# Optimization experiments

Hardware: AMD Instinct MI355X
Metric: run time of the kernel (lower is better)

## Reference

```python
import jax, jax.numpy as jnp
import numpy as np
from jax import lax

N, OC, IC, K = 32, 256, 256, 3
H = W = 56
STRIDE = 1
PADDING = 1
SPARSITY = 0.9  # fraction of zero weights


def setup_inputs() -> dict:
    key = jax.random.key(0)
    k_in, k_w, k_b, k_m = jax.random.split(key, 4)
    input = jax.random.normal(k_in, (N, IC, H, W), dtype=jnp.float32)
    weight = jax.random.normal(k_w, (OC, IC, K, K), dtype=jnp.float32) * 0.05
    bias = jax.random.normal(k_b, (OC,), dtype=jnp.float32) * 0.05
    mask = jax.random.bernoulli(k_m, p=1.0 - SPARSITY, shape=(OC, IC, K, K))
    return {"input": input, "weight": weight, "bias": bias, "mask": mask}


def reference(input, weight, bias, mask):
    # SparseConv2d stores only nonzero weights (W_val at W_idx); mathematically this
    # is a dense conv2d with the masked weight tensor.
    w = jnp.where(mask, weight, jnp.zeros((), dtype=weight.dtype))
    out = lax.conv_general_dilated(
        input, w,
        window_strides=(STRIDE, STRIDE),
        padding=[(PADDING, PADDING), (PADDING, PADDING)],
        dimension_numbers=("NCHW", "OIHW", "NCHW"),
    )
    return out + bias[None, :, None, None]
```

## Files before the change

kernel.cpp:

```cpp
#include <hip/hip_runtime.h>

constexpr int NB=32, ICC=256, OCC=256, HH=56, WW=56;
constexpr int HW=HH*WW, CHW=ICC*HW;
constexpr int YT=14, MT=2;
constexpr int BUFB = 6*56*64;
constexpr int ZOFF = 2*BUFB;
constexpr int LROW=58;
constexpr int PAD=36;
constexpr int LDS_ELEMS=6*LROW*PAD;

using short8  = __attribute__((ext_vector_type(8))) short;
using short4v = __attribute__((ext_vector_type(4))) short;
using f32x4   = __attribute__((ext_vector_type(4))) float;

__device__ inline unsigned bf16rne(float x){
  unsigned u = __float_as_uint(x);
  return (u + 0x7fffu + ((u>>16)&1u)) >> 16;
}

__global__ __launch_bounds__(256) void pack_weights(
    const float* __restrict__ w, const int* __restrict__ mask,
    unsigned short* __restrict__ wb){
  const int oc = blockIdx.x, ic = threadIdx.x;
  const int base = (oc*ICC + ic)*9;
  #pragma unroll
  for (int j=0;j<9;++j){
    float v = (mask[base+j] != 0) ? w[base+j] : 0.f;
    wb[(j*OCC + oc)*ICC + ic] = (unsigned short)bf16rne(v);
  }
}

__global__ __launch_bounds__(256) void pack_input(
    const float* __restrict__ in, unsigned short* __restrict__ inb){
  __shared__ unsigned short t[56*258];
  const int bid = blockIdx.x;
  const int n = bid/56, y = bid - n*56;
  const float* src = in + (size_t)n*CHW + y*WW;
  const int tid = threadIdx.x;
  #pragma unroll
  for (int i=0;i<14;++i){
    int idx = tid + i*256;
    int ic = idx / 14, xg = idx - ic*14;
    float4 v = *(const float4*)(src + ic*HW + xg*4);
    int xb = xg*4;
    t[(xb+0)*258 + ic] = (unsigned short)bf16rne(v.x);
    t[(xb+1)*258 + ic] = (unsigned short)bf16rne(v.y);
    t[(xb+2)*258 + ic] = (unsigned short)bf16rne(v.z);
    t[(xb+3)*258 + ic] = (unsigned short)bf16rne(v.w);
  }
  __syncthreads();
  unsigned* dst = (unsigned*)(inb + (size_t)(n*56+y)*56*256);
  #pragma unroll
  for (int i=0;i<28;++i){
    int idx = tid + i*256;
    int x = idx >> 7, icp = idx & 127;
    dst[idx] = *(const unsigned*)&t[x*258 + icp*2];
  }
}

__global__ __launch_bounds__(256,2) void conv_mfma(
    const unsigned short* __restrict__ inb, const unsigned short* __restrict__ wb,
    const float* __restrict__ bias, float* __restrict__ out){
  __shared__ unsigned short xt[(2*BUFB + 16)/2];

  const int lid  = blockIdx.x;
  const int xcd  = lid & 7, slot = lid >> 3;
  const int ngrp = slot / 28, rem = slot - ngrp*28;
  const int mt   = rem / 14,  yt  = rem - mt*14;
  const int n    = xcd + 8*ngrp;
  const int y0   = yt*4, ocb = mt*128;

  const int tid  = threadIdx.x;
  const int lane = tid & 63, wv = tid >> 6;
  const int q    = lane >> 4, l16 = lane & 15;

  const int ocw = ocb + (wv & 1)*64;
  const int pxw = (wv >> 1)*112;

  int xp[7], yl[7];
  #pragma unroll
  for (int p=0;p<7;++p){
    int px = pxw + p*16 + l16;
    yl[p] = px / 56;  xp[p] = px - yl[p]*56;
  }

  f32x4 acc[4][7];
  #pragma unroll
  for (int s=0;s<4;++s)
    #pragma unroll
    for (int p=0;p<7;++p) acc[s][p] = (f32x4){0.f,0.f,0.f,0.f};

  if (tid == 0) *(f32x4*)((char*)xt + ZOFF) = (f32x4){0.f,0.f,0.f,0.f};

  const unsigned short* nb = inb + (size_t)n*(56*56*256);

  auto stage = [&](int buf, int ch){
    const int ic0 = ch*32;
    #pragma unroll
    for (int i=0;i<6;++i){
      int idx = tid + i*256;
      if (idx < 1344){
        int r   = idx / 224;
        int rm  = idx - r*224;
        int cc  = rm >> 2, sub = rm & 3;
        int y   = y0 - 1 + r;
        y = y < 0 ? 0 : (y > 55 ? 55 : y);
        int icg = sub ^ ((cc>>1)&3);
        const unsigned short* gp = nb + (y*56 + cc)*256 + ic0 + icg*8;
        char* lp = (char*)xt + buf*BUFB + idx*16;
        __builtin_amdgcn_global_load_lds(
            (const __attribute__((address_space(1))) void*)gp,
            (__attribute__((address_space(3))) void*)lp, 16, 0, 0);
      }
    }
  };

  auto compute = [&](int buf, int ch){
    const int ic0 = ch*32;
    const char* xb = (const char*)xt + buf*BUFB;
    const char* zp = (const char*)xt + ZOFF;
    #pragma unroll
    for (int kh=0;kh<3;++kh){
      #pragma unroll
      for (int kw=0;kw<3;++kw){
        const int j = kh*3 + kw;
        const unsigned short* wp = wb + (j*OCC + ocw + l16)*ICC + ic0 + q*8;
        short8 a0 = *(const short8*)(wp          );
        short8 a1 = *(const short8*)(wp + 16*ICC );
        short8 a2 = *(const short8*)(wp + 32*ICC );
        short8 a3 = *(const short8*)(wp + 48*ICC );
        #pragma unroll
        for (int p=0;p<7;++p){
          int xq = xp[p] + kw - 1;
          int yq = y0 - 1 + yl[p] + kh;
          bool valid = ((unsigned)xq < 56u) & ((unsigned)yq < 56u);
          int addr = (((yl[p]+kh)*56 + xq)<<6) + ((q ^ ((xq>>1)&3))<<4);
          const char* bp = valid ? (xb + addr) : zp;
          short8 b = *(const short8*)bp;
          acc[0][p] = __builtin_amdgcn_mfma_f32_16x16x32_bf16(a0, b, acc[0][p], 0,0,0);
          acc[1][p] = __builtin_amdgcn_mfma_f32_16x16x32_bf16(a1, b, acc[1][p], 0,0,0);
          acc[2][p] = __builtin_amdgcn_mfma_f32_16x16x32_bf16(a2, b, acc[2][p], 0,0,0);
          acc[3][p] = __builtin_amdgcn_mfma_f32_16x16x32_bf16(a3, b, acc[3][p], 0,0,0);
        }
      }
    }
  };

  stage(0, 0);
  __syncthreads();

  for (int ch=0; ch<8; ++ch){
    if (ch < 7) stage((ch+1)&1, ch+1);
    compute(ch&1, ch);
    __syncthreads();
  }

  #pragma unroll
  for (int s=0;s<4;++s){
    const int oc4 = ocw + s*16 + q*4;
    float4 bv = *(const float4*)(bias + oc4);
    #pragma unroll
    for (int i=0;i<4;++i){
      const float bb = (i==0)?bv.x:(i==1)?bv.y:(i==2)?bv.z:bv.w;
      float* op = out + (n*OCC + oc4 + i)*HW + y0*WW + pxw + l16;
      #pragma unroll
      for (int p=0;p<7;++p){
        op[p*16] = acc[s][p][i] + bb;
      }
    }
  }
}

__global__ __launch_bounds__(256,2) void conv_mfma_f32(
    const float* __restrict__ in, const unsigned short* __restrict__ wb,
    const float* __restrict__ bias, float* __restrict__ out){
  __shared__ unsigned short xt[LDS_ELEMS];

  const int lid  = blockIdx.x;
  const int xcd  = lid & 7, slot = lid >> 3;
  const int ngrp = slot / 28, rem = slot - ngrp*28;
  const int mt   = rem / 14,  yt  = rem - mt*14;
  const int n    = xcd + 8*ngrp;
  const int y0   = yt*4, ocb = mt*128;

  const int tid  = threadIdx.x;
  const int lane = tid & 63, wv = tid >> 6;
  const int q    = lane >> 4, l16 = lane & 15;

  for (int i = tid; i < LDS_ELEMS/2; i += 256) ((unsigned*)xt)[i] = 0u;

  const int ocw = ocb + (wv & 1)*64;
  const int pxw = (wv >> 1)*112;

  int pbase[7];
  #pragma unroll
  for (int p=0;p<7;++p){
    int px = pxw + p*16 + l16;
    int ylv = px / 56, x = px - ylv*56;
    pbase[p] = (ylv*LROW + x)*(PAD*2) + q*16;
  }

  f32x4 acc[4][7];
  #pragma unroll
  for (int s=0;s<4;++s)
    #pragma unroll
    for (int p=0;p<7;++p) acc[s][p] = (f32x4){0.f,0.f,0.f,0.f};

  const int rskipA = (yt==0)      ? 0 : -1;
  const int rskipB = (yt==YT-1)   ? 5 : -1;

  __syncthreads();

  for (int ch=0; ch<8; ++ch){
    const int ic0 = ch*32;
    #pragma unroll
    for (int i=0;i<6;++i){
      int idx = tid + i*256;
      if (idx < 1344){
        int r  = idx / 224;
        int r2 = idx - r*224;
        int xg = r2 >> 4, icp = r2 & 15;
        if (r != rskipA && r != rskipB){
          int y = y0 - 1 + r;
          const float* gp = in + n*CHW + (ic0 + icp*2)*HW + y*WW + xg*4;
          float4 g0 = *(const float4*)gp;
          float4 g1 = *(const float4*)(gp + HW);
          unsigned w0 = bf16rne(g0.x) | (bf16rne(g1.x)<<16);
          unsigned w1 = bf16rne(g0.y) | (bf16rne(g1.y)<<16);
          unsigned w2 = bf16rne(g0.z) | (bf16rne(g1.z)<<16);
          unsigned w3 = bf16rne(g0.w) | (bf16rne(g1.w)<<16);
          unsigned* dp = (unsigned*)xt + (r*LROW + 1 + xg*4)*(PAD/2) + icp;
          dp[0]         = w0;
          dp[PAD/2]     = w1;
          dp[PAD]       = w2;
          dp[3*(PAD/2)] = w3;
        }
      }
    }
    __syncthreads();

    #pragma unroll
    for (int kh=0;kh<3;++kh){
      #pragma unroll
      for (int kw=0;kw<3;++kw){
        const int j = kh*3 + kw;
        const unsigned short* wp = wb + (j*OCC + ocw + l16)*ICC + ic0 + q*8;
        short8 a0 = *(const short8*)(wp          );
        short8 a1 = *(const short8*)(wp + 16*ICC );
        short8 a2 = *(const short8*)(wp + 32*ICC );
        short8 a3 = *(const short8*)(wp + 48*ICC );
        const int doff = (kh*LROW + kw)*(PAD*2);
        #pragma unroll
        for (int p=0;p<7;++p){
          const char* bp = (const char*)xt + pbase[p] + doff;
          short4v blo = *(const short4v*)(bp    );
          short4v bhi = *(const short4v*)(bp + 8);
          short8 b = __builtin_shufflevector(blo, bhi, 0,1,2,3,4,5,6,7);
          acc[0][p] = __builtin_amdgcn_mfma_f32_16x16x32_bf16(a0, b, acc[0][p], 0,0,0);
          acc[1][p] = __builtin_amdgcn_mfma_f32_16x16x32_bf16(a1, b, acc[1][p], 0,0,0);
          acc[2][p] = __builtin_amdgcn_mfma_f32_16x16x32_bf16(a2, b, acc[2][p], 0,0,0);
          acc[3][p] = __builtin_amdgcn_mfma_f32_16x16x32_bf16(a3, b, acc[3][p], 0,0,0);
        }
      }
    }
    __syncthreads();
  }

  #pragma unroll
  for (int s=0;s<4;++s){
    const int oc4 = ocw + s*16 + q*4;
    float4 bv = *(const float4*)(bias + oc4);
    #pragma unroll
    for (int i=0;i<4;++i){
      const float bb = (i==0)?bv.x:(i==1)?bv.y:(i==2)?bv.z:bv.w;
      float* op = out + (n*OCC + oc4 + i)*HW + y0*WW + pxw + l16;
      #pragma unroll
      for (int p=0;p<7;++p){
        op[p*16] = acc[s][p][i] + bb;
      }
    }
  }
}

extern "C" void kernel_launch(void* const* d_in, const int* in_sizes, int n_in,
                              void* d_out, int out_size, void* d_ws, size_t ws_size,
                              hipStream_t stream) {
  const float* in   = (const float*)d_in[0];
  const float* w    = (const float*)d_in[1];
  const float* bias = (const float*)d_in[2];
  const int*   mask = (const int*)d_in[3];
  float*       out  = (float*)d_out;
  unsigned short* wb = (unsigned short*)d_ws;

  const size_t WB_BYTES  = (size_t)9*OCC*ICC*2;
  const size_t INB_BYTES = (size_t)NB*HH*WW*ICC*2;

  pack_weights<<<OCC, 256, 0, stream>>>(w, mask, wb);
  if (ws_size >= WB_BYTES + INB_BYTES){
    unsigned short* inb = (unsigned short*)((char*)d_ws + WB_BYTES);
    pack_input<<<NB*HH, 256, 0, stream>>>(in, inb);
    conv_mfma<<<8*4*MT*YT, 256, 0, stream>>>(inb, wb, bias, out);
  } else {
    conv_mfma_f32<<<8*4*MT*YT, 256, 0, stream>>>(in, wb, bias, out);
  }
}
```

Baseline: 345.8 us.

## Use zero-padded LDS halo tile and prefetch next tap weights in conv MFMA

```diff
diff --git a/kernel.cpp b/kernel.cpp
--- a/kernel.cpp
+++ b/kernel.cpp
@@ -2,9 +2,8 @@
 
 constexpr int NB=32, ICC=256, OCC=256, HH=56, WW=56;
 constexpr int HW=HH*WW, CHW=ICC*HW;
-constexpr int YT=14, MT=2;
-constexpr int BUFB = 6*56*64;
-constexpr int ZOFF = 2*BUFB;
+constexpr int YT=14;
+constexpr int BUFB = 6*58*64;
 constexpr int LROW=58;
 constexpr int PAD=36;
 constexpr int LDS_ELEMS=6*LROW*PAD;
@@ -61,7 +60,7 @@
 __global__ __launch_bounds__(256,2) void conv_mfma(
     const unsigned short* __restrict__ inb, const unsigned short* __restrict__ wb,
     const float* __restrict__ bias, float* __restrict__ out){
-  __shared__ unsigned short xt[(2*BUFB + 16)/2];
+  __shared__ unsigned short xt[2*6*58*32];
 
   const int lid  = blockIdx.x;
   const int xcd  = lid & 7, slot = lid >> 3;
@@ -77,11 +76,12 @@
   const int ocw = ocb + (wv & 1)*64;
   const int pxw = (wv >> 1)*112;
 
-  int xp[7], yl[7];
+  int cellbase[7];
   #pragma unroll
   for (int p=0;p<7;++p){
     int px = pxw + p*16 + l16;
-    yl[p] = px / 56;  xp[p] = px - yl[p]*56;
+    int yl = px / 56, x = px - yl*56;
+    cellbase[p] = (yl*58 + x)*64 + q*16;
   }
 
   f32x4 acc[4][7];
@@ -90,7 +90,8 @@
     #pragma unroll
     for (int p=0;p<7;++p) acc[s][p] = (f32x4){0.f,0.f,0.f,0.f};
 
-  if (tid == 0) *(f32x4*)((char*)xt + ZOFF) = (f32x4){0.f,0.f,0.f,0.f};
+  const int rskipA = (yt==0)      ? 0 : -1;
+  const int rskipB = (yt==YT-1)   ? 5 : -1;
 
   const unsigned short* nb = inb + (size_t)n*(56*56*256);
 
@@ -98,19 +99,18 @@
     const int ic0 = ch*32;
     #pragma unroll
     for (int i=0;i<6;++i){
-      int idx = tid + i*256;
-      if (idx < 1344){
-        int r   = idx / 224;
-        int rm  = idx - r*224;
-        int cc  = rm >> 2, sub = rm & 3;
-        int y   = y0 - 1 + r;
-        y = y < 0 ? 0 : (y > 55 ? 55 : y);
-        int icg = sub ^ ((cc>>1)&3);
-        const unsigned short* gp = nb + (y*56 + cc)*256 + ic0 + icg*8;
-        char* lp = (char*)xt + buf*BUFB + idx*16;
-        __builtin_amdgcn_global_load_lds(
-            (const __attribute__((address_space(1))) void*)gp,
-            (__attribute__((address_space(3))) void*)lp, 16, 0, 0);
+      int t   = wv*6 + i;
+      int row = t >> 2, k = t & 3;
+      if (row != rskipA && row != rskipB){
+        int ir = k*64 + lane;
+        int cc = ir >> 2, sub = ir & 3;
+        int y  = y0 - 1 + row;
+        const unsigned short* gp = nb + (y*56 + cc)*256 + ic0 + sub*8;
+        char* lp = (char*)xt + buf*BUFB + (row*58 + 1)*64 + k*1024 + lane*16;
+        if (ir < 224)
+          __builtin_amdgcn_global_load_lds(
+              (const __attribute__((address_space(1))) void*)gp,
+              (__attribute__((address_space(3))) void*)lp, 16, 0, 0);
       }
     }
   };
@@ -118,33 +118,39 @@
   auto compute = [&](int buf, int ch){
     const int ic0 = ch*32;
     const char* xb = (const char*)xt + buf*BUFB;
-    const char* zp = (const char*)xt + ZOFF;
-    #pragma unroll
-    for (int kh=0;kh<3;++kh){
+    const unsigned short* wpb = wb + (ocw + l16)*ICC + ic0 + q*8;
+    short8 a0 = *(const short8*)(wpb          );
+    short8 a1 = *(const short8*)(wpb + 16*ICC );
+    short8 a2 = *(const short8*)(wpb + 32*ICC );
+    short8 a3 = *(const short8*)(wpb + 48*ICC );
+    __builtin_amdgcn_s_setprio(1);
+    #pragma unroll
+    for (int j=0;j<9;++j){
+      short8 n0, n1, n2, n3;
+      if (j < 8){
+        const unsigned short* wn = wpb + (j+1)*OCC*ICC;
+        n0 = *(const short8*)(wn          );
+        n1 = *(const short8*)(wn + 16*ICC );
+        n2 = *(const short8*)(wn + 32*ICC );
+        n3 = *(const short8*)(wn + 48*ICC );
+      }
+      const int kh = j/3, kw = j - kh*3;
+      const int doff = (kh*58 + kw)*64;
       #pragma unroll
-      for (int kw=0;kw<3;++kw){
-        const int j = kh*3 + kw;
-        const unsigned short* wp = wb + (j*OCC + ocw + l16)*ICC + ic0 + q*8;
-        short8 a0 = *(const short8*)(wp          );
-        short8 a1 = *(const short8*)(wp + 16*ICC );
-        short8 a2 = *(const short8*)(wp + 32*ICC );
-        short8 a3 = *(const short8*)(wp + 48*ICC );
-        #pragma unroll
-        for (int p=0;p<7;++p){
-          int xq = xp[p] + kw - 1;
-          int yq = y0 - 1 + yl[p] + kh;
-          bool valid = ((unsigned)xq < 56u) & ((unsigned)yq < 56u);
-          int addr = (((yl[p]+kh)*56 + xq)<<6) + ((q ^ ((xq>>1)&3))<<4);
-          const char* bp = valid ? (xb + addr) : zp;
-          short8 b = *(const short8*)bp;
-          acc[0][p] = __builtin_amdgcn_mfma_f32_16x16x32_bf16(a0, b, acc[0][p], 0,0,0);
-          acc[1][p] = __builtin_amdgcn_mfma_f32_16x16x32_bf16(a1, b, acc[1][p], 0,0,0);
-          acc[2][p] = __builtin_amdgcn_mfma_f32_16x16x32_bf16(a2, b, acc[2][p], 0,0,0);
-          acc[3][p] = __builtin_amdgcn_mfma_f32_16x16x32_bf16(a3, b, acc[3][p], 0,0,0);
-        }
-      }
-    }
+      for (int p=0;p<7;++p){
+        short8 b = *(const short8*)(xb + cellbase[p] + doff);
+        acc[0][p] = __builtin_amdgcn_mfma_f32_16x16x32_bf16(a0, b, acc[0][p], 0,0,0);
+        acc[1][p] = __builtin_amdgcn_mfma_f32_16x16x32_bf16(a1, b, acc[1][p], 0,0,0);
+        acc[2][p] = __builtin_amdgcn_mfma_f32_16x16x32_bf16(a2, b, acc[2][p], 0,0,0);
+        acc[3][p] = __builtin_amdgcn_mfma_f32_16x16x32_bf16(a3, b, acc[3][p], 0,0,0);
+      }
+      if (j < 8){ a0=n0; a1=n1; a2=n2; a3=n3; }
+    }
+    __builtin_amdgcn_s_setprio(0);
   };
+
+  for (int i = tid; i < 2*BUFB/4; i += 256) ((unsigned*)xt)[i] = 0u;
+  __syncthreads();
 
   stage(0, 0);
   __syncthreads();
@@ -299,8 +305,8 @@
   if (ws_size >= WB_BYTES + INB_BYTES){
     unsigned short* inb = (unsigned short*)((char*)d_ws + WB_BYTES);
     pack_input<<<NB*HH, 256, 0, stream>>>(in, inb);
-    conv_mfma<<<8*4*MT*YT, 256, 0, stream>>>(inb, wb, bias, out);
+    conv_mfma<<<8*4*2*YT, 256, 0, stream>>>(inb, wb, bias, out);
   } else {
-    conv_mfma_f32<<<8*4*MT*YT, 256, 0, stream>>>(in, wb, bias, out);
-  }
-}
+    conv_mfma_f32<<<8*4*2*YT, 256, 0, stream>>>(in, wb, bias, out);
+  }
+}
```

New measurement: 345.8 us. About the same (+0.0%).
